# Performance work log

Hardware: AMD Instinct MI355X
Metric: run time of the kernel (lower is better)

The kernel has to match this reference:

```python
import jax, jax.numpy as jnp
import numpy as np

D = 256      # d_model
H = 8        # n_heads
L = 4        # n_levels
P = 4        # n_points
DFF = 1024   # d_ffn
DH = D // H  # head dim
SPATIAL = np.array([[100, 100], [50, 50], [25, 25], [13, 13]], dtype=np.int64)  # (H_l, W_l)
LV = int((SPATIAL[:, 0] * SPATIAL[:, 1]).sum())  # 13294 flattened memory tokens


def layer_norm(x, w, b, eps=1e-5):
    m = jnp.mean(x, -1, keepdims=True)
    v = jnp.mean((x - m) ** 2, -1, keepdims=True)
    return (x - m) * jax.lax.rsqrt(v + eps) * w + b


def setup_inputs() -> dict:
    key = jax.random.key(0)
    ks = jax.random.split(key, 16)
    nq, bs = 900, 8

    def w(k, shape, s=0.02):
        return jax.random.normal(k, shape, dtype=jnp.float32) * s

    return {
        "tgt": jax.random.normal(ks[0], (nq, bs, D), jnp.float32),
        "tgt_query_pos": jax.random.normal(ks[1], (nq, bs, D), jnp.float32),
        "tgt_reference_points": jax.random.uniform(ks[2], (nq, bs, L, 2), jnp.float32),
        "memory": jax.random.normal(ks[3], (LV, bs, D), jnp.float32),
        "sa_Wqkv": w(ks[4], (3 * D, D)), "sa_bqkv": jnp.zeros((3 * D,), jnp.float32),
        "sa_Wo": w(ks[5], (D, D)), "sa_bo": jnp.zeros((D,), jnp.float32),
        "ln1_w": jnp.ones((D,), jnp.float32), "ln1_b": jnp.zeros((D,), jnp.float32),
        "ln2_w": jnp.ones((D,), jnp.float32), "ln2_b": jnp.zeros((D,), jnp.float32),
        "ln3_w": jnp.ones((D,), jnp.float32), "ln3_b": jnp.zeros((D,), jnp.float32),
        "ca_Woff": w(ks[6], (H * L * P * 2, D)), "ca_boff": w(ks[7], (H * L * P * 2,), 0.5),
        "ca_Wattn": w(ks[8], (H * L * P, D)), "ca_battn": jnp.zeros((H * L * P,), jnp.float32),
        "ca_Wval": w(ks[9], (D, D)), "ca_bval": jnp.zeros((D,), jnp.float32),
        "ca_Wout": w(ks[10], (D, D)), "ca_bout": jnp.zeros((D,), jnp.float32),
        "ffn_W1": w(ks[11], (DFF, D)), "ffn_b1": jnp.zeros((DFF,), jnp.float32),
        "ffn_W2": w(ks[12], (D, DFF)), "ffn_b2": jnp.zeros((D,), jnp.float32),
        "memory_key_padding_mask": jnp.zeros((bs, LV), jnp.bool_),
        "memory_spatial_shapes": jnp.asarray(SPATIAL),
    }


def msdeform_attn(query, ref, value, mask, shapes_np,
                  Woff, boff, Wattn, battn, Wval, bval, Wout, bout):
    # query: [bs,nq,D], ref: [bs,nq,L,2], value: [bs,lv,D], mask: [bs,lv]
    bs, nq, _ = query.shape
    lv = value.shape[1]
    v = value @ Wval.T + bval
    v = jnp.where(mask[:, :, None], 0.0, v)
    v = v.reshape(bs, lv, H, DH).transpose(0, 2, 1, 3)  # [bs,H,lv,DH]
    off = (query @ Woff.T + boff).reshape(bs, nq, H, L, P, 2)
    aw = jax.nn.softmax((query @ Wattn.T + battn).reshape(bs, nq, H, L * P), -1)
    aw = aw.reshape(bs, nq, H, L, P)
    # offset normalizer is [W_l, H_l]
    norm = jnp.asarray(shapes_np[:, ::-1].copy(), jnp.float32)  # [L,2]
    loc = ref[:, :, None, :, None, :] + off / norm[None, None, None, :, None, :]
    out = jnp.zeros((bs, nq, H, DH), jnp.float32)
    start = 0
    for l in range(L):
        Hl, Wl = int(shapes_np[l, 0]), int(shapes_np[l, 1])
        vf = v[:, :, start:start + Hl * Wl]  # [bs,H,Hl*Wl,DH]
        start += Hl * Wl
        # grid_sample(align_corners=False) pixel coords
        x = loc[:, :, :, l, :, 0] * Wl - 0.5  # [bs,nq,H,P]
        y = loc[:, :, :, l, :, 1] * Hl - 0.5
        x0 = jnp.floor(x); y0 = jnp.floor(y)
        fx = x - x0; fy = y - y0
        x0i = x0.astype(jnp.int32); y0i = y0.astype(jnp.int32)

        def gather(yi, xi):
            valid = ((xi >= 0) & (xi < Wl) & (yi >= 0) & (yi < Hl)).astype(jnp.float32)
            idx = jnp.clip(yi, 0, Hl - 1) * Wl + jnp.clip(xi, 0, Wl - 1)
            idx_t = idx.transpose(0, 2, 1, 3).reshape(bs, H, nq * P, 1)
            g = jnp.take_along_axis(vf, idx_t, axis=2)  # [bs,H,nq*P,DH]
            return g * valid.transpose(0, 2, 1, 3).reshape(bs, H, nq * P, 1)

        def wgt(w):
            return w.transpose(0, 2, 1, 3).reshape(bs, H, nq * P, 1)

        samp = (gather(y0i, x0i) * wgt((1 - fx) * (1 - fy))
                + gather(y0i, x0i + 1) * wgt(fx * (1 - fy))
                + gather(y0i + 1, x0i) * wgt((1 - fx) * fy)
                + gather(y0i + 1, x0i + 1) * wgt(fx * fy))
        samp = samp.reshape(bs, H, nq, P, DH)
        out = out + jnp.einsum('bhqpd,bqhp->bqhd', samp, aw[:, :, :, l])
    return out.reshape(bs, nq, D) @ Wout.T + bout


def reference(tgt, tgt_query_pos, tgt_reference_points, memory,
              sa_Wqkv, sa_bqkv, sa_Wo, sa_bo,
              ln1_w, ln1_b, ln2_w, ln2_b, ln3_w, ln3_b,
              ca_Woff, ca_boff, ca_Wattn, ca_battn, ca_Wval, ca_bval, ca_Wout, ca_bout,
              ffn_W1, ffn_b1, ffn_W2, ffn_b2,
              memory_key_padding_mask, memory_spatial_shapes):
    shapes_np = np.asarray(memory_spatial_shapes)  # static per trace
    nq, bs, _ = tgt.shape
    # --- self attention (post-LN, residual) ---
    q = tgt + tgt_query_pos
    qp = (q @ sa_Wqkv[:D].T + sa_bqkv[:D]).reshape(nq, bs, H, DH)
    kp = (q @ sa_Wqkv[D:2 * D].T + sa_bqkv[D:2 * D]).reshape(nq, bs, H, DH)
    vp = (tgt @ sa_Wqkv[2 * D:].T + sa_bqkv[2 * D:]).reshape(nq, bs, H, DH)
    scores = jnp.einsum('qbhd,kbhd->bhqk', qp, kp) * (1.0 / float(np.sqrt(DH)))
    attn = jax.nn.softmax(scores, -1)
    o = jnp.einsum('bhqk,kbhd->qbhd', attn, vp).reshape(nq, bs, D) @ sa_Wo.T + sa_bo
    tgt = layer_norm(tgt + o, ln2_w, ln2_b)
    # --- multi-scale deformable cross attention ---
    query = (tgt + tgt_query_pos).transpose(1, 0, 2)      # [bs,nq,D]
    ref = tgt_reference_points.transpose(1, 0, 2, 3)      # [bs,nq,L,2]
    val = memory.transpose(1, 0, 2)                       # [bs,lv,D]
    ca = msdeform_attn(query, ref, val, memory_key_padding_mask, shapes_np,
                       ca_Woff, ca_boff, ca_Wattn, ca_battn,
                       ca_Wval, ca_bval, ca_Wout, ca_bout).transpose(1, 0, 2)
    tgt = layer_norm(tgt + ca, ln1_w, ln1_b)
    # --- FFN ---
    t2 = jax.nn.relu(tgt @ ffn_W1.T + ffn_b1) @ ffn_W2.T + ffn_b2
    return layer_norm(tgt + t2, ln3_w, ln3_b)
```

## Files before the change

kernel.cpp:

```cpp
#include <hip/hip_runtime.h>
#include <hip/hip_bf16.h>

#define NQ   900
#define BSZ  8
#define DM   256
#define NH   8
#define DHD  32
#define DFF_ 1024
#define LVTOT 13294
#define NTOK (NQ*BSZ)
#define MVAL (LVTOT*BSZ)

typedef __attribute__((ext_vector_type(8))) short bf16x8;
typedef __attribute__((ext_vector_type(4))) short bf16x4;
typedef __attribute__((ext_vector_type(4))) float f32x4;
typedef unsigned int u32;

__device__ __forceinline__ unsigned short f2bf(float x) {
  union { __hip_bfloat16 h; unsigned short u; } cv;
  cv.h = __float2bfloat16(x);
  return cv.u;
}
__device__ __forceinline__ float bf2f(unsigned short u) {
  union { __hip_bfloat16 h; unsigned short u; } cv;
  cv.u = u;
  return __bfloat162float(cv.h);
}

__device__ __forceinline__ void gl_lds16(const void* gsrc, void* ldst) {
  __builtin_amdgcn_global_load_lds(
      (const __attribute__((address_space(1))) u32*)gsrc,
      (__attribute__((address_space(3))) u32*)ldst, 16, 0, 0);
}

__global__ __launch_bounds__(256) void prep_kernel(
    const float* p0, const float* p1, const float* p2, const float* p3,
    const float* p4, const float* p5, const float* p6, const float* p7,
    unsigned short* wdst,
    const float* a, const float* b, unsigned short* qdst,
    const float* boff, const float* battn, float* bcat) {
  int bid = blockIdx.x, tid = threadIdx.x;
  if (bid < 496) {
    long i8 = ((long)bid * 256 + tid) * 8;
    const float* src; long off;
    if      (i8 < 196608) { src = p0; off = i8; }
    else if (i8 < 262144) { src = p1; off = i8 - 196608; }
    else if (i8 < 327680) { src = p2; off = i8 - 262144; }
    else if (i8 < 393216) { src = p3; off = i8 - 327680; }
    else if (i8 < 425984) { src = p4; off = i8 - 393216; }
    else if (i8 < 491520) { src = p5; off = i8 - 425984; }
    else if (i8 < 753664) { src = p6; off = i8 - 491520; }
    else                  { src = p7; off = i8 - 753664; }
    float4 x = *(const float4*)(src + off);
    float4 y = *(const float4*)(src + off + 4);
    bf16x8 v;
    v[0] = (short)f2bf(x.x); v[1] = (short)f2bf(x.y);
    v[2] = (short)f2bf(x.z); v[3] = (short)f2bf(x.w);
    v[4] = (short)f2bf(y.x); v[5] = (short)f2bf(y.y);
    v[6] = (short)f2bf(y.z); v[7] = (short)f2bf(y.w);
    *(bf16x8*)(wdst + i8) = v;
  } else if (bid < 496 + 900) {
    int i = (bid - 496) * 256 + tid;
    float4 a0 = ((const float4*)a)[i * 2], a1 = ((const float4*)a)[i * 2 + 1];
    float4 b0 = ((const float4*)b)[i * 2], b1 = ((const float4*)b)[i * 2 + 1];
    bf16x8 v;
    v[0] = (short)f2bf(a0.x + b0.x); v[1] = (short)f2bf(a0.y + b0.y);
    v[2] = (short)f2bf(a0.z + b0.z); v[3] = (short)f2bf(a0.w + b0.w);
    v[4] = (short)f2bf(a1.x + b1.x); v[5] = (short)f2bf(a1.y + b1.y);
    v[6] = (short)f2bf(a1.z + b1.z); v[7] = (short)f2bf(a1.w + b1.w);
    *(bf16x8*)(qdst + (long)i * 8) = v;
  } else {
    int i = (bid - 1396) * 256 + tid;
    if (i < 256) bcat[i] = boff[i];
    else if (i < 384) bcat[i] = battn[i - 256];
  }
}

struct B3 {
  const void* A[3];
  const unsigned short* W[3];
  const float* bias[3];
  void* C[3];
  int M[3], ldc[3], af32[3], blk0[3], nx[3];
};

__global__ __launch_bounds__(256, 4) void gemm_batch3_kernel(B3 ops) {
  constexpr int K = 256, NSTEP = 4;
  __shared__ alignas(16) unsigned char As[32768];
  __shared__ alignas(16) unsigned char Bs[16384];
  int bid = blockIdx.x;
  int oi = (bid >= ops.blk0[2]) ? 2 : (bid >= ops.blk0[1] ? 1 : 0);
  int rel = bid - ops.blk0[oi];
  int nx = ops.nx[oi];
  int bx = rel % nx, by = rel / nx;
  const void* Araw = ops.A[oi];
  const unsigned short* W = ops.W[oi];
  const float* bias = ops.bias[oi];
  void* C = ops.C[oi];
  int M = ops.M[oi], ldc = ops.ldc[oi], AF32 = ops.af32[oi];

  int tid = threadIdx.x;
  int l = tid & 63, w = tid >> 6;
  int lr = l & 15, lg = l >> 4;
  int wr = w >> 1, wc = w & 1;
  int n0 = bx * 128, m0 = by * 128;
  int phase = by & (NSTEP - 1);

  f32x4 acc[4][4];
#pragma unroll
  for (int m = 0; m < 4; m++)
#pragma unroll
    for (int n = 0; n < 4; n++) acc[m][n] = (f32x4){0.f, 0.f, 0.f, 0.f};

  for (int tt = 0; tt < NSTEP; tt++) {
    int t = tt + phase; if (t >= NSTEP) t -= NSTEP;
    int k0 = t * 64;
    __syncthreads();
#pragma unroll
    for (int i4 = 0; i4 < 4; i4++) {
      int i = i4 * 4 + w;
      int row = i * 8 + (l >> 3);
      int sc = (l & 7) ^ (row & 7);
      gl_lds16(W + (long)(n0 + row) * K + k0 + sc * 8, Bs + i * 1024 + l * 16);
    }
    if (AF32) {
      const float* Af = (const float*)Araw;
#pragma unroll
      for (int i4 = 0; i4 < 8; i4++) {
        int i = i4 * 4 + w;
        int row = i * 4 + (l >> 4);
        int g = m0 + row; if (g >= M) g = M - 1;
        int sc = (l & 15) ^ (row & 15);
        gl_lds16(Af + (long)g * K + k0 + sc * 4, As + i * 1024 + l * 16);
      }
    } else {
      const unsigned short* A = (const unsigned short*)Araw;
#pragma unroll
      for (int i4 = 0; i4 < 4; i4++) {
        int i = i4 * 4 + w;
        int row = i * 8 + (l >> 3);
        int g = m0 + row; if (g >= M) g = M - 1;
        int sc = (l & 7) ^ (row & 7);
        gl_lds16(A + (long)g * K + k0 + sc * 8, As + i * 1024 + l * 16);
      }
    }
    __syncthreads();
#pragma unroll
    for (int sk = 0; sk < 2; sk++) {
      bf16x8 af[4], bfr[4];
      if (AF32) {
#pragma unroll
        for (int m = 0; m < 4; m++) {
          int row = wr * 64 + m * 16 + lr;
          int ca = (sk * 8 + lg * 2) ^ (row & 15);
          int cb = (sk * 8 + lg * 2 + 1) ^ (row & 15);
          f32x4 fa = *(const f32x4*)(As + row * 256 + ca * 16);
          f32x4 fb = *(const f32x4*)(As + row * 256 + cb * 16);
          bf16x8 v;
          v[0] = (short)f2bf(fa[0]); v[1] = (short)f2bf(fa[1]);
          v[2] = (short)f2bf(fa[2]); v[3] = (short)f2bf(fa[3]);
          v[4] = (short)f2bf(fb[0]); v[5] = (short)f2bf(fb[1]);
          v[6] = (short)f2bf(fb[2]); v[7] = (short)f2bf(fb[3]);
          af[m] = v;
        }
      } else {
#pragma unroll
        for (int m = 0; m < 4; m++) {
          int row = wr * 64 + m * 16 + lr;
          int c = (sk * 4 + lg) ^ (row & 7);
          af[m] = *(const bf16x8*)(As + row * 128 + c * 16);
        }
      }
#pragma unroll
      for (int n = 0; n < 4; n++) {
        int row = wc * 64 + n * 16 + lr;
        int c = (sk * 4 + lg) ^ (row & 7);
        bfr[n] = *(const bf16x8*)(Bs + row * 128 + c * 16);
      }
#pragma unroll
      for (int m = 0; m < 4; m++)
#pragma unroll
        for (int n = 0; n < 4; n++)
          acc[m][n] = __builtin_amdgcn_mfma_f32_16x16x32_bf16(af[m], bfr[n], acc[m][n], 0, 0, 0);
    }
  }

  float bv[4];
#pragma unroll
  for (int ni = 0; ni < 4; ni++) bv[ni] = bias[n0 + wc * 64 + ni * 16 + lr];
#pragma unroll
  for (int mi = 0; mi < 4; mi++) {
#pragma unroll
    for (int r = 0; r < 4; r++) {
      int row = m0 + wr * 64 + mi * 16 + lg * 4 + r;
      if (row < M) {
#pragma unroll
        for (int ni = 0; ni < 4; ni++) {
          int col = n0 + wc * 64 + ni * 16 + lr;
          ((unsigned short*)C)[(long)row * ldc + col] = f2bf(acc[mi][ni][r] + bv[ni]);
        }
      }
    }
  }
}

template <int AF32, int OUT_BF16, int RELU, int NSTEP>
__global__ __launch_bounds__(256, 4) void gemm_s_kernel(
    const void* __restrict__ Araw, const unsigned short* __restrict__ W,
    const float* __restrict__ bias, void* __restrict__ C,
    int M, int ldc) {
  constexpr int K = NSTEP * 64;
  constexpr int ABYTES = AF32 ? 32768 : 16384;
  __shared__ alignas(16) unsigned char As[ABYTES];
  __shared__ alignas(16) unsigned char Bs[16384];
  int tid = threadIdx.x;
  int l = tid & 63, w = tid >> 6;
  int lr = l & 15, lg = l >> 4;
  int wr = w >> 1, wc = w & 1;
  int n0 = blockIdx.x * 128, m0 = blockIdx.y * 128;
  int phase = blockIdx.y & (NSTEP - 1);

  f32x4 acc[4][4];
#pragma unroll
  for (int m = 0; m < 4; m++)
#pragma unroll
    for (int n = 0; n < 4; n++) acc[m][n] = (f32x4){0.f, 0.f, 0.f, 0.f};

  for (int tt = 0; tt < NSTEP; tt++) {
    int t = tt + phase; if (t >= NSTEP) t -= NSTEP;
    int k0 = t * 64;
    __syncthreads();
#pragma unroll
    for (int i4 = 0; i4 < 4; i4++) {
      int i = i4 * 4 + w;
      int row = i * 8 + (l >> 3);
      int sc = (l & 7) ^ (row & 7);
      gl_lds16(W + (long)(n0 + row) * K + k0 + sc * 8, Bs + i * 1024 + l * 16);
    }
    if (AF32) {
      const float* Af = (const float*)Araw;
#pragma unroll
      for (int i4 = 0; i4 < 8; i4++) {
        int i = i4 * 4 + w;
        int row = i * 4 + (l >> 4);
        int g = m0 + row; if (g >= M) g = M - 1;
        int sc = (l & 15) ^ (row & 15);
        gl_lds16(Af + (long)g * K + k0 + sc * 4, As + i * 1024 + l * 16);
      }
    } else {
      const unsigned short* A = (const unsigned short*)Araw;
#pragma unroll
      for (int i4 = 0; i4 < 4; i4++) {
        int i = i4 * 4 + w;
        int row = i * 8 + (l >> 3);
        int g = m0 + row; if (g >= M) g = M - 1;
        int sc = (l & 7) ^ (row & 7);
        gl_lds16(A + (long)g * K + k0 + sc * 8, As + i * 1024 + l * 16);
      }
    }
    __syncthreads();
#pragma unroll
    for (int sk = 0; sk < 2; sk++) {
      bf16x8 af[4], bfr[4];
      if (AF32) {
#pragma unroll
        for (int m = 0; m < 4; m++) {
          int row = wr * 64 + m * 16 + lr;
          int ca = (sk * 8 + lg * 2) ^ (row & 15);
          int cb = (sk * 8 + lg * 2 + 1) ^ (row & 15);
          f32x4 fa = *(const f32x4*)(As + row * 256 + ca * 16);
          f32x4 fb = *(const f32x4*)(As + row * 256 + cb * 16);
          bf16x8 v;
          v[0] = (short)f2bf(fa[0]); v[1] = (short)f2bf(fa[1]);
          v[2] = (short)f2bf(fa[2]); v[3] = (short)f2bf(fa[3]);
          v[4] = (short)f2bf(fb[0]); v[5] = (short)f2bf(fb[1]);
          v[6] = (short)f2bf(fb[2]); v[7] = (short)f2bf(fb[3]);
          af[m] = v;
        }
      } else {
#pragma unroll
        for (int m = 0; m < 4; m++) {
          int row = wr * 64 + m * 16 + lr;
          int c = (sk * 4 + lg) ^ (row & 7);
          af[m] = *(const bf16x8*)(As + row * 128 + c * 16);
        }
      }
#pragma unroll
      for (int n = 0; n < 4; n++) {
        int row = wc * 64 + n * 16 + lr;
        int c = (sk * 4 + lg) ^ (row & 7);
        bfr[n] = *(const bf16x8*)(Bs + row * 128 + c * 16);
      }
#pragma unroll
      for (int m = 0; m < 4; m++)
#pragma unroll
        for (int n = 0; n < 4; n++)
          acc[m][n] = __builtin_amdgcn_mfma_f32_16x16x32_bf16(af[m], bfr[n], acc[m][n], 0, 0, 0);
    }
  }

  float bv[4];
#pragma unroll
  for (int ni = 0; ni < 4; ni++) bv[ni] = bias[n0 + wc * 64 + ni * 16 + lr];
#pragma unroll
  for (int mi = 0; mi < 4; mi++) {
#pragma unroll
    for (int r = 0; r < 4; r++) {
      int row = m0 + wr * 64 + mi * 16 + lg * 4 + r;
      if (row < M) {
#pragma unroll
        for (int ni = 0; ni < 4; ni++) {
          int col = n0 + wc * 64 + ni * 16 + lr;
          float v = acc[mi][ni][r] + bv[ni];
          if (RELU) v = fmaxf(v, 0.f);
          if (OUT_BF16) ((unsigned short*)C)[(long)row * ldc + col] = f2bf(v);
          else          ((float*)C)[(long)row * ldc + col] = v;
        }
      }
    }
  }
}

__global__ __launch_bounds__(256) void attn_mfma_kernel(const unsigned short* __restrict__ qkv,
                                                        unsigned short* __restrict__ out) {
  __shared__ unsigned short Vt[32][72];
  __shared__ unsigned short Ps[4][16][72];
  int tid = threadIdx.x;
  int l = tid & 63, w = tid >> 6;
  int lr = l & 15, lg = l >> 4;
  int bid = blockIdx.x;
  int xcd = bid & 7;
  int rest = bid >> 3;
  int pgrp = rest / 15;
  int qt   = rest - pgrp * 15;
  int pair = pgrp * 8 + xcd;
  int q0 = qt * 64;
  int h = pair & 7, b = pair >> 3;
  const float scale = 0.17677669529663687f;

  int qrow = q0 + w * 16 + lr;
  int qclamp = qrow < 899 ? qrow : 899;
  bf16x8 qf = *(const bf16x8*)(qkv + ((long)qclamp * 8 + b) * 768 + h * 32 + lg * 8);

  f32x4 o_acc[2];
  o_acc[0] = (f32x4){0.f, 0.f, 0.f, 0.f};
  o_acc[1] = (f32x4){0.f, 0.f, 0.f, 0.f};
  float m_run[4] = {-1e30f, -1e30f, -1e30f, -1e30f};
  float l_run[4] = {0.f, 0.f, 0.f, 0.f};

  for (int k0 = 0; k0 < NQ; k0 += 64) {
    __syncthreads();
    {
      int key = tid >> 2, dg = tid & 3;
      int kk = k0 + key; if (kk > 899) kk = 899;
      bf16x8 vv = *(const bf16x8*)(qkv + ((long)kk * 8 + b) * 768 + 512 + h * 32 + dg * 8);
#pragma unroll
      for (int j = 0; j < 8; j++) Vt[dg * 8 + j][key] = (unsigned short)vv[j];
    }
    f32x4 sg[4];
#pragma unroll
    for (int ng = 0; ng < 4; ng++) {
      int key = k0 + ng * 16 + lr; int kc = key < 899 ? key : 899;
      bf16x8 kf = *(const bf16x8*)(qkv + ((long)kc * 8 + b) * 768 + 256 + h * 32 + lg * 8);
      sg[ng] = __builtin_amdgcn_mfma_f32_16x16x32_bf16(qf, kf, (f32x4){0.f, 0.f, 0.f, 0.f}, 0, 0, 0);
    }
    float sv[4][4];
#pragma unroll
    for (int ng = 0; ng < 4; ng++) {
      bool bad = (k0 + ng * 16 + lr) >= NQ;
#pragma unroll
      for (int r = 0; r < 4; r++) sv[ng][r] = bad ? -1e30f : sg[ng][r] * scale;
    }
    float p[4][4];
#pragma unroll
    for (int r = 0; r < 4; r++) {
      float rmax = fmaxf(fmaxf(sv[0][r], sv[1][r]), fmaxf(sv[2][r], sv[3][r]));
#pragma unroll
      for (int mk = 8; mk; mk >>= 1) rmax = fmaxf(rmax, __shfl_xor(rmax, mk));
      float mnew = fmaxf(m_run[r], rmax);
      float fs = __expf(m_run[r] - mnew);
      m_run[r] = mnew;
      float ps = 0.f;
#pragma unroll
      for (int ng = 0; ng < 4; ng++) { p[ng][r] = __expf(sv[ng][r] - mnew); ps += p[ng][r]; }
#pragma unroll
      for (int mk = 8; mk; mk >>= 1) ps += __shfl_xor(ps, mk);
      l_run[r] = l_run[r] * fs + ps;
      o_acc[0][r] *= fs;
      o_acc[1][r] *= fs;
    }
#pragma unroll
    for (int ng = 0; ng < 4; ng++)
#pragma unroll
      for (int r = 0; r < 4; r++)
        Ps[w][lg * 4 + r][lr + ng * 16] = f2bf(p[ng][r]);
    __syncthreads();
#pragma unroll
    for (int ks = 0; ks < 2; ks++) {
      bf16x8 pf = *(const bf16x8*)&Ps[w][lr][ks * 32 + lg * 8];
#pragma unroll
      for (int ni = 0; ni < 2; ni++) {
        bf16x8 vf = *(const bf16x8*)&Vt[ni * 16 + lr][ks * 32 + lg * 8];
        o_acc[ni] = __builtin_amdgcn_mfma_f32_16x16x32_bf16(pf, vf, o_acc[ni], 0, 0, 0);
      }
    }
  }
#pragma unroll
  for (int r = 0; r < 4; r++) {
    int orow = q0 + w * 16 + lg * 4 + r;
    if (orow < NQ) {
      float inv = 1.f / l_run[r];
      unsigned short* op = out + ((long)orow * 8 + b) * 256 + h * 32 + lr;
      op[0]  = f2bf(o_acc[0][r] * inv);
      op[16] = f2bf(o_acc[1][r] * inv);
    }
  }
}

__device__ __forceinline__ void fetch16_acc(const unsigned short* __restrict__ vtmp, int lo, int W,
                                            int yi, int xi, int b, int col0, float wgt,
                                            float* a) {
  if ((xi < 0) | (xi >= W) | (yi < 0) | (yi >= W)) return;
  const unsigned short* p = vtmp + ((long)((lo + yi * W + xi) * BSZ + b)) * 256 + col0;
  bf16x8 r0 = *(const bf16x8*)p;
  bf16x8 r1 = *(const bf16x8*)(p + 8);
#pragma unroll
  for (int j = 0; j < 8; j++) a[j] += wgt * bf2f((unsigned short)r0[j]);
#pragma unroll
  for (int j = 0; j < 8; j++) a[8 + j] += wgt * bf2f((unsigned short)r1[j]);
}

__global__ __launch_bounds__(256) void sampler_kernel(const unsigned short* __restrict__ vtmp,
                                                      const float* __restrict__ oa,
                                                      const float* __restrict__ ref,
                                                      unsigned short* __restrict__ samp) {
  __shared__ float s_off[16][256];
  __shared__ float s_aw[16][128];
  __shared__ float s_ref[16][8];
  int tid = threadIdx.x;
  int bid = blockIdx.x;
  int img = bid & 7;
  int jb  = bid >> 3;
  int qi0 = jb * 16;
#pragma unroll
  for (int k = 0; k < 16; k++) {
    int qi = qi0 + k; if (qi > 899) qi = 899;
    long t = (long)qi * 8 + img;
    s_off[k][tid] = oa[t * 384 + tid];
  }
#pragma unroll
  for (int i = 0; i < 8; i++) {
    int idx = i * 256 + tid;
    int k = idx >> 7, c = idx & 127;
    int qi = qi0 + k; if (qi > 899) qi = 899;
    long t = (long)qi * 8 + img;
    s_aw[k][c] = oa[t * 384 + 256 + c];
  }
  if (tid < 128) {
    int k = tid >> 3;
    int qi = qi0 + k; if (qi > 899) qi = 899;
    long t = (long)qi * 8 + img;
    s_ref[k][tid & 7] = ref[t * 8 + (tid & 7)];
  }
  __syncthreads();
  if (tid < 128) {
    int k = tid >> 3, hh = tid & 7;
    float* p = &s_aw[k][hh * 16];
    float m = -1e30f;
#pragma unroll
    for (int j = 0; j < 16; j++) m = fmaxf(m, p[j]);
    float s = 0.f;
#pragma unroll
    for (int j = 0; j < 16; j++) { p[j] = __expf(p[j] - m); s += p[j]; }
    float inv = 1.f / s;
#pragma unroll
    for (int j = 0; j < 16; j++) p[j] *= inv;
  }
  __syncthreads();
  int w = tid >> 4;
  int l = tid & 15;
  int qi = qi0 + w;
  int h = l >> 1, col0 = h * 32 + (l & 1) * 16;
  int b = img;
  const int Wls[4]  = {100, 50, 25, 13};
  const int lofs[4] = {0, 10000, 12500, 13125};
  float a[16];
#pragma unroll
  for (int j = 0; j < 16; j++) a[j] = 0.f;
#pragma unroll
  for (int lvl = 0; lvl < 4; lvl++) {
    int W = Wls[lvl];
    float Wf = (float)W;
    int lo = lofs[lvl];
    float rx = s_ref[w][lvl * 2 + 0], ry = s_ref[w][lvl * 2 + 1];
#pragma unroll
    for (int p = 0; p < 4; p++) {
      float ox = s_off[w][((h * 4 + lvl) * 4 + p) * 2 + 0];
      float oy = s_off[w][((h * 4 + lvl) * 4 + p) * 2 + 1];
      float x = rx * Wf + ox - 0.5f;
      float y = ry * Wf + oy - 0.5f;
      float x0f = floorf(x), y0f = floorf(y);
      float fx = x - x0f, fy = y - y0f;
      int x0 = (int)x0f, y0 = (int)y0f;
      float aa = s_aw[w][h * 16 + lvl * 4 + p];
      float w00 = aa * (1.f - fx) * (1.f - fy);
      float w01 = aa * fx * (1.f - fy);
      float w10 = aa * (1.f - fx) * fy;
      float w11 = aa * fx * fy;
      fetch16_acc(vtmp, lo, W, y0,     x0,     b, col0, w00, a);
      fetch16_acc(vtmp, lo, W, y0,     x0 + 1, b, col0, w01, a);
      fetch16_acc(vtmp, lo, W, y0 + 1, x0,     b, col0, w10, a);
      fetch16_acc(vtmp, lo, W, y0 + 1, x0 + 1, b, col0, w11, a);
    }
  }
  if (qi < NQ) {
    long t = (long)qi * 8 + img;
    bf16x8 o0, o1;
#pragma unroll
    for (int j = 0; j < 8; j++) { o0[j] = (short)f2bf(a[j]); o1[j] = (short)f2bf(a[8 + j]); }
    *(bf16x8*)(samp + t * 256 + col0) = o0;
    *(bf16x8*)(samp + t * 256 + col0 + 8) = o1;
  }
}

__global__ __launch_bounds__(256) void ln_kernel(const float* __restrict__ x,
                                                 const float* __restrict__ res,
                                                 const float* __restrict__ w,
                                                 const float* __restrict__ bvec,
                                                 float* __restrict__ out,
                                                 unsigned short* __restrict__ out_bf,
                                                 const float* __restrict__ pos,
                                                 unsigned short* __restrict__ pos_bf,
                                                 int rows) {
  int wv = threadIdx.x >> 6, lane = threadIdx.x & 63;
  int row = blockIdx.x * 4 + wv;
  if (row >= rows) return;
  float4 xv = *(const float4*)(x + (long)row * 256 + lane * 4);
  float4 rv = *(const float4*)(res + (long)row * 256 + lane * 4);
  float v0 = xv.x + rv.x, v1 = xv.y + rv.y, v2 = xv.z + rv.z, v3 = xv.w + rv.w;
  float s = v0 + v1 + v2 + v3;
#pragma unroll
  for (int o = 32; o; o >>= 1) s += __shfl_xor(s, o);
  float mean = s * (1.f / 256.f);
  float d0 = v0 - mean, d1 = v1 - mean, d2 = v2 - mean, d3 = v3 - mean;
  float q = d0 * d0 + d1 * d1 + d2 * d2 + d3 * d3;
#pragma unroll
  for (int o = 32; o; o >>= 1) q += __shfl_xor(q, o);
  float rstd = rsqrtf(q * (1.f / 256.f) + 1e-5f);
  float4 wv4 = *(const float4*)(w + lane * 4);
  float4 bv4 = *(const float4*)(bvec + lane * 4);
  float o0 = d0 * rstd * wv4.x + bv4.x;
  float o1 = d1 * rstd * wv4.y + bv4.y;
  float o2 = d2 * rstd * wv4.z + bv4.z;
  float o3 = d3 * rstd * wv4.w + bv4.w;
  *(float4*)(out + (long)row * 256 + lane * 4) = make_float4(o0, o1, o2, o3);
  if (out_bf) {
    unsigned short* p = out_bf + (long)row * 256 + lane * 4;
    p[0] = f2bf(o0); p[1] = f2bf(o1); p[2] = f2bf(o2); p[3] = f2bf(o3);
  }
  if (pos_bf) {
    float4 pv = *(const float4*)(pos + (long)row * 256 + lane * 4);
    unsigned short* p = pos_bf + (long)row * 256 + lane * 4;
    p[0] = f2bf(o0 + pv.x); p[1] = f2bf(o1 + pv.y);
    p[2] = f2bf(o2 + pv.z); p[3] = f2bf(o3 + pv.w);
  }
}

extern "C" void kernel_launch(void* const* d_in, const int* in_sizes, int n_in,
                              void* d_out, int out_size, void* d_ws, size_t ws_size,
                              hipStream_t stream) {
  const float* tgt     = (const float*)d_in[0];
  const float* pos     = (const float*)d_in[1];
  const float* refpts  = (const float*)d_in[2];
  const float* memory  = (const float*)d_in[3];
  const float* sa_Wqkv = (const float*)d_in[4];
  const float* sa_bqkv = (const float*)d_in[5];
  const float* sa_Wo   = (const float*)d_in[6];
  const float* sa_bo   = (const float*)d_in[7];
  const float* ln1_w   = (const float*)d_in[8];
  const float* ln1_b   = (const float*)d_in[9];
  const float* ln2_w   = (const float*)d_in[10];
  const float* ln2_b   = (const float*)d_in[11];
  const float* ln3_w   = (const float*)d_in[12];
  const float* ln3_b   = (const float*)d_in[13];
  const float* ca_Woff = (const float*)d_in[14];
  const float* ca_boff = (const float*)d_in[15];
  const float* ca_Wattn= (const float*)d_in[16];
  const float* ca_battn= (const float*)d_in[17];
  const float* ca_Wval = (const float*)d_in[18];
  const float* ca_bval = (const float*)d_in[19];
  const float* ca_Wout = (const float*)d_in[20];
  const float* ca_bout = (const float*)d_in[21];
  const float* ffn_W1  = (const float*)d_in[22];
  const float* ffn_b1  = (const float*)d_in[23];
  const float* ffn_W2  = (const float*)d_in[24];
  const float* ffn_b2  = (const float*)d_in[25];

  char* ws = (char*)d_ws;
  float*          buf_ca = (float*)(ws);
  float*          buf_t3 = (float*)(ws + 8388608);
  unsigned short* t3_bf  = (unsigned short*)(ws + 16777216);
  unsigned short* buf_h  = (unsigned short*)(ws + 20971520);
  float*          buf_f  = (float*)(ws + 36700160);
  float*          bias_cat = (float*)(ws + 44072960);
  unsigned short* buf_v  = (unsigned short*)(ws + 54452224);
  unsigned short* wts    = (unsigned short*)(ws + 112590848);
  unsigned short* buf_q  = (unsigned short*)(ws + 114622464);
  unsigned short* buf_qkv= (unsigned short*)(ws + 118308864);
  float*          buf_oa = (float*)(ws + 118308864);
  unsigned short* buf_o  = (unsigned short*)(ws + 129368064);
  unsigned short* buf_smp= (unsigned short*)(ws + 129368064);
  float*          buf_t2 = (float*)(ws + 133054464);

  const unsigned short* w_qkv = wts + 0;
  const unsigned short* w_o   = wts + 196608;
  const unsigned short* w_val = wts + 262144;
  const unsigned short* w_oa  = wts + 327680;
  const unsigned short* w_out = wts + 425984;
  const unsigned short* w_f1  = wts + 491520;
  const unsigned short* w_f2  = wts + 753664;

  dim3 blk(256);

  prep_kernel<<<1398, blk, 0, stream>>>(sa_Wqkv, sa_Wo, ca_Wval, ca_Woff, ca_Wattn,
                                        ca_Wout, ffn_W1, ffn_W2, wts,
                                        tgt, pos, buf_q, ca_boff, ca_battn, bias_cat);

  B3 ops;
  ops.A[0] = memory;   ops.W[0] = w_val;           ops.bias[0] = ca_bval;      ops.C[0] = buf_v;
  ops.M[0] = MVAL;     ops.ldc[0] = 256;           ops.af32[0] = 1;            ops.nx[0] = 2;
  ops.A[1] = buf_q;    ops.W[1] = w_qkv;           ops.bias[1] = sa_bqkv;      ops.C[1] = buf_qkv;
  ops.M[1] = NTOK;     ops.ldc[1] = 768;           ops.af32[1] = 0;            ops.nx[1] = 4;
  ops.A[2] = tgt;      ops.W[2] = w_qkv + 512*256; ops.bias[2] = sa_bqkv + 512; ops.C[2] = buf_qkv + 512;
  ops.M[2] = NTOK;     ops.ldc[2] = 768;           ops.af32[2] = 1;            ops.nx[2] = 2;
  ops.blk0[0] = 0; ops.blk0[1] = 1662; ops.blk0[2] = 1890;
  gemm_batch3_kernel<<<2004, blk, 0, stream>>>(ops);

  attn_mfma_kernel<<<960, blk, 0, stream>>>(buf_qkv, buf_o);
  gemm_s_kernel<0, 0, 0, 4><<<dim3(2, 57), blk, 0, stream>>>(buf_o, w_o, sa_bo,
                                                             buf_t2, NTOK, 256);
  ln_kernel<<<1800, blk, 0, stream>>>(buf_t2, tgt, ln2_w, ln2_b, buf_t2, nullptr,
                                      pos, buf_q, NTOK);
  gemm_s_kernel<0, 0, 0, 4><<<dim3(3, 57), blk, 0, stream>>>(buf_q, w_oa, bias_cat,
                                                             buf_oa, NTOK, 384);
  sampler_kernel<<<456, blk, 0, stream>>>(buf_v, buf_oa, refpts, buf_smp);
  gemm_s_kernel<0, 0, 0, 4><<<dim3(2, 57), blk, 0, stream>>>(buf_smp, w_out, ca_bout,
                                                             buf_ca, NTOK, 256);
  ln_kernel<<<1800, blk, 0, stream>>>(buf_ca, buf_t2, ln1_w, ln1_b, buf_t3, t3_bf,
                                      nullptr, nullptr, NTOK);
  gemm_s_kernel<0, 1, 1, 4><<<dim3(8, 57), blk, 0, stream>>>(t3_bf, w_f1, ffn_b1,
                                                             buf_h, NTOK, 1024);
  gemm_s_kernel<0, 0, 0, 16><<<dim3(2, 57), blk, 0, stream>>>(buf_h, w_f2, ffn_b2,
                                                              buf_f, NTOK, 256);
  ln_kernel<<<1800, blk, 0, stream>>>(buf_f, buf_t3, ln3_w, ln3_b, (float*)d_out, nullptr,
                                      nullptr, nullptr, NTOK);
}
```

Baseline: 213.6 us.

## Fuse value projection GEMM with self-attention into one heterogeneous launch

The large memory value-projection GEMM moves out of the batched QKV GEMM launch into a new combined kernel. Its first 1662 blocks run the value GEMM and the remaining 960 blocks run the self-attention, which does not depend on it. The batched launch shrinks to just the Q/K and V projections, so attention can start sooner and overlap with the big value GEMM instead of waiting behind it. The cost is a shared 48KB LDS footprint for attention blocks, which may reduce their occupancy, and block scheduling order now decides how much overlap actually happens.

Result: slower. 221.9 us (+3.9%).

```diff
diff --git a/kernel.cpp b/kernel.cpp
--- a/kernel.cpp
+++ b/kernel.cpp
@@ -204,6 +204,192 @@
   }
 }
 
+#define NVB 1662
+__global__ __launch_bounds__(256, 4) void value_attn_kernel(
+    const float* __restrict__ memory, const unsigned short* __restrict__ Wv,
+    const float* __restrict__ bval, unsigned short* __restrict__ Cv,
+    const unsigned short* __restrict__ qkv, unsigned short* __restrict__ out) {
+  __shared__ alignas(16) unsigned char smem[49152];
+  int tid = threadIdx.x;
+  int l = tid & 63, w = tid >> 6;
+  int lr = l & 15, lg = l >> 4;
+
+  if (blockIdx.x < NVB) {
+    constexpr int K = 256, NSTEP = 4;
+    unsigned char* As = smem;
+    unsigned char* Bs = smem + 32768;
+    int wr = w >> 1, wc = w & 1;
+    int bx = blockIdx.x & 1, by = blockIdx.x >> 1;
+    int n0 = bx * 128, m0 = by * 128;
+    int phase = by & (NSTEP - 1);
+
+    f32x4 acc[4][4];
+#pragma unroll
+    for (int m = 0; m < 4; m++)
+#pragma unroll
+      for (int n = 0; n < 4; n++) acc[m][n] = (f32x4){0.f, 0.f, 0.f, 0.f};
+
+    for (int tt = 0; tt < NSTEP; tt++) {
+      int t = tt + phase; if (t >= NSTEP) t -= NSTEP;
+      int k0 = t * 64;
+      __syncthreads();
+#pragma unroll
+      for (int i4 = 0; i4 < 4; i4++) {
+        int i = i4 * 4 + w;
+        int row = i * 8 + (l >> 3);
+        int sc = (l & 7) ^ (row & 7);
+        gl_lds16(Wv + (long)(n0 + row) * K + k0 + sc * 8, Bs + i * 1024 + l * 16);
+      }
+#pragma unroll
+      for (int i4 = 0; i4 < 8; i4++) {
+        int i = i4 * 4 + w;
+        int row = i * 4 + (l >> 4);
+        int g = m0 + row; if (g >= MVAL) g = MVAL - 1;
+        int sc = (l & 15) ^ (row & 15);
+        gl_lds16(memory + (long)g * K + k0 + sc * 4, As + i * 1024 + l * 16);
+      }
+      __syncthreads();
+#pragma unroll
+      for (int sk = 0; sk < 2; sk++) {
+        bf16x8 af[4], bfr[4];
+#pragma unroll
+        for (int m = 0; m < 4; m++) {
+          int row = wr * 64 + m * 16 + lr;
+          int ca = (sk * 8 + lg * 2) ^ (row & 15);
+          int cb = (sk * 8 + lg * 2 + 1) ^ (row & 15);
+          f32x4 fa = *(const f32x4*)(As + row * 256 + ca * 16);
+          f32x4 fb = *(const f32x4*)(As + row * 256 + cb * 16);
+          bf16x8 v;
+          v[0] = (short)f2bf(fa[0]); v[1] = (short)f2bf(fa[1]);
+          v[2] = (short)f2bf(fa[2]); v[3] = (short)f2bf(fa[3]);
+          v[4] = (short)f2bf(fb[0]); v[5] = (short)f2bf(fb[1]);
+          v[6] = (short)f2bf(fb[2]); v[7] = (short)f2bf(fb[3]);
+          af[m] = v;
+        }
+#pragma unroll
+        for (int n = 0; n < 4; n++) {
+          int row = wc * 64 + n * 16 + lr;
+          int c = (sk * 4 + lg) ^ (row & 7);
+          bfr[n] = *(const bf16x8*)(Bs + row * 128 + c * 16);
+        }
+#pragma unroll
+        for (int m = 0; m < 4; m++)
+#pragma unroll
+          for (int n = 0; n < 4; n++)
+            acc[m][n] = __builtin_amdgcn_mfma_f32_16x16x32_bf16(af[m], bfr[n], acc[m][n], 0, 0, 0);
+      }
+    }
+
+    float bv[4];
+#pragma unroll
+    for (int ni = 0; ni < 4; ni++) bv[ni] = bval[n0 + wc * 64 + ni * 16 + lr];
+#pragma unroll
+    for (int mi = 0; mi < 4; mi++) {
+#pragma unroll
+      for (int r = 0; r < 4; r++) {
+        int row = m0 + wr * 64 + mi * 16 + lg * 4 + r;
+        if (row < MVAL) {
+#pragma unroll
+          for (int ni = 0; ni < 4; ni++) {
+            int col = n0 + wc * 64 + ni * 16 + lr;
+            Cv[(long)row * 256 + col] = f2bf(acc[mi][ni][r] + bv[ni]);
+          }
+        }
+      }
+    }
+  } else {
+    unsigned short (*Vt)[72] = (unsigned short(*)[72])smem;
+    unsigned short (*Ps)[16][72] = (unsigned short(*)[16][72])(smem + 4608);
+    int bid = blockIdx.x - NVB;
+    int xcd = bid & 7;
+    int rest = bid >> 3;
+    int pgrp = rest / 15;
+    int qt   = rest - pgrp * 15;
+    int pair = pgrp * 8 + xcd;
+    int q0 = qt * 64;
+    int h = pair & 7, b = pair >> 3;
+    const float scale = 0.17677669529663687f;
+
+    int qrow = q0 + w * 16 + lr;
+    int qclamp = qrow < 899 ? qrow : 899;
+    bf16x8 qf = *(const bf16x8*)(qkv + ((long)qclamp * 8 + b) * 768 + h * 32 + lg * 8);
+
+    f32x4 o_acc[2];
+    o_acc[0] = (f32x4){0.f, 0.f, 0.f, 0.f};
+    o_acc[1] = (f32x4){0.f, 0.f, 0.f, 0.f};
+    float m_run[4] = {-1e30f, -1e30f, -1e30f, -1e30f};
+    float l_run[4] = {0.f, 0.f, 0.f, 0.f};
+
+    for (int k0 = 0; k0 < NQ; k0 += 64) {
+      __syncthreads();
+      {
+        int key = tid >> 2, dg = tid & 3;
+        int kk = k0 + key; if (kk > 899) kk = 899;
+        bf16x8 vv = *(const bf16x8*)(qkv + ((long)kk * 8 + b) * 768 + 512 + h * 32 + dg * 8);
+#pragma unroll
+        for (int j = 0; j < 8; j++) Vt[dg * 8 + j][key] = (unsigned short)vv[j];
+      }
+      f32x4 sg[4];
+#pragma unroll
+      for (int ng = 0; ng < 4; ng++) {
+        int key = k0 + ng * 16 + lr; int kc = key < 899 ? key : 899;
+        bf16x8 kf = *(const bf16x8*)(qkv + ((long)kc * 8 + b) * 768 + 256 + h * 32 + lg * 8);
+        sg[ng] = __builtin_amdgcn_mfma_f32_16x16x32_bf16(qf, kf, (f32x4){0.f, 0.f, 0.f, 0.f}, 0, 0, 0);
+      }
+      float sv[4][4];
+#pragma unroll
+      for (int ng = 0; ng < 4; ng++) {
+        bool bad = (k0 + ng * 16 + lr) >= NQ;
+#pragma unroll
+        for (int r = 0; r < 4; r++) sv[ng][r] = bad ? -1e30f : sg[ng][r] * scale;
+      }
+      float p[4][4];
+#pragma unroll
+      for (int r = 0; r < 4; r++) {
+        float rmax = fmaxf(fmaxf(sv[0][r], sv[1][r]), fmaxf(sv[2][r], sv[3][r]));
+#pragma unroll
+        for (int mk = 8; mk; mk >>= 1) rmax = fmaxf(rmax, __shfl_xor(rmax, mk));
+        float mnew = fmaxf(m_run[r], rmax);
+        float fs = __expf(m_run[r] - mnew);
+        m_run[r] = mnew;
+        float ps = 0.f;
+#pragma unroll
+        for (int ng = 0; ng < 4; ng++) { p[ng][r] = __expf(sv[ng][r] - mnew); ps += p[ng][r]; }
+#pragma unroll
+        for (int mk = 8; mk; mk >>= 1) ps += __shfl_xor(ps, mk);
+        l_run[r] = l_run[r] * fs + ps;
+        o_acc[0][r] *= fs;
+        o_acc[1][r] *= fs;
+      }
+#pragma unroll
+      for (int ng = 0; ng < 4; ng++)
+#pragma unroll
+        for (int r = 0; r < 4; r++)
+          Ps[w][lg * 4 + r][lr + ng * 16] = f2bf(p[ng][r]);
+      __syncthreads();
+#pragma unroll
+      for (int ks = 0; ks < 2; ks++) {
+        bf16x8 pf = *(const bf16x8*)&Ps[w][lr][ks * 32 + lg * 8];
+#pragma unroll
+        for (int ni = 0; ni < 2; ni++) {
+          bf16x8 vf = *(const bf16x8*)&Vt[ni * 16 + lr][ks * 32 + lg * 8];
+          o_acc[ni] = __builtin_amdgcn_mfma_f32_16x16x32_bf16(pf, vf, o_acc[ni], 0, 0, 0);
+        }
+      }
+    }
+#pragma unroll
+    for (int r = 0; r < 4; r++) {
+      int orow = q0 + w * 16 + lg * 4 + r;
+      if (orow < NQ) {
+        float inv = 1.f / l_run[r];
+        unsigned short* op = out + ((long)orow * 8 + b) * 256 + h * 32 + lr;
+        op[0]  = f2bf(o_acc[0][r] * inv);
+        op[16] = f2bf(o_acc[1][r] * inv);
+      }
+    }
+  }
+}
+
 template <int AF32, int OUT_BF16, int RELU, int NSTEP>
 __global__ __launch_bounds__(256, 4) void gemm_s_kernel(
     const void* __restrict__ Araw, const unsigned short* __restrict__ W,
@@ -317,102 +503,6 @@
           else          ((float*)C)[(long)row * ldc + col] = v;
         }
       }
-    }
-  }
-}
-
-__global__ __launch_bounds__(256) void attn_mfma_kernel(const unsigned short* __restrict__ qkv,
-                                                        unsigned short* __restrict__ out) {
-  __shared__ unsigned short Vt[32][72];
-  __shared__ unsigned short Ps[4][16][72];
-  int tid = threadIdx.x;
-  int l = tid & 63, w = tid >> 6;
-  int lr = l & 15, lg = l >> 4;
-  int bid = blockIdx.x;
-  int xcd = bid & 7;
-  int rest = bid >> 3;
-  int pgrp = rest / 15;
-  int qt   = rest - pgrp * 15;
-  int pair = pgrp * 8 + xcd;
-  int q0 = qt * 64;
-  int h = pair & 7, b = pair >> 3;
-  const float scale = 0.17677669529663687f;
-
-  int qrow = q0 + w * 16 + lr;
-  int qclamp = qrow < 899 ? qrow : 899;
-  bf16x8 qf = *(const bf16x8*)(qkv + ((long)qclamp * 8 + b) * 768 + h * 32 + lg * 8);
-
-  f32x4 o_acc[2];
-  o_acc[0] = (f32x4){0.f, 0.f, 0.f, 0.f};
-  o_acc[1] = (f32x4){0.f, 0.f, 0.f, 0.f};
-  float m_run[4] = {-1e30f, -1e30f, -1e30f, -1e30f};
-  float l_run[4] = {0.f, 0.f, 0.f, 0.f};
-
-  for (int k0 = 0; k0 < NQ; k0 += 64) {
-    __syncthreads();
-    {
-      int key = tid >> 2, dg = tid & 3;
-      int kk = k0 + key; if (kk > 899) kk = 899;
-      bf16x8 vv = *(const bf16x8*)(qkv + ((long)kk * 8 + b) * 768 + 512 + h * 32 + dg * 8);
-#pragma unroll
-      for (int j = 0; j < 8; j++) Vt[dg * 8 + j][key] = (unsigned short)vv[j];
-    }
-    f32x4 sg[4];
-#pragma unroll
-    for (int ng = 0; ng < 4; ng++) {
-      int key = k0 + ng * 16 + lr; int kc = key < 899 ? key : 899;
-      bf16x8 kf = *(const bf16x8*)(qkv + ((long)kc * 8 + b) * 768 + 256 + h * 32 + lg * 8);
-      sg[ng] = __builtin_amdgcn_mfma_f32_16x16x32_bf16(qf, kf, (f32x4){0.f, 0.f, 0.f, 0.f}, 0, 0, 0);
-    }
-    float sv[4][4];
-#pragma unroll
-    for (int ng = 0; ng < 4; ng++) {
-      bool bad = (k0 + ng * 16 + lr) >= NQ;
-#pragma unroll
-      for (int r = 0; r < 4; r++) sv[ng][r] = bad ? -1e30f : sg[ng][r] * scale;
-    }
-    float p[4][4];
-#pragma unroll
-    for (int r = 0; r < 4; r++) {
-      float rmax = fmaxf(fmaxf(sv[0][r], sv[1][r]), fmaxf(sv[2][r], sv[3][r]));
-#pragma unroll
-      for (int mk = 8; mk; mk >>= 1) rmax = fmaxf(rmax, __shfl_xor(rmax, mk));
-      float mnew = fmaxf(m_run[r], rmax);
-      float fs = __expf(m_run[r] - mnew);
-      m_run[r] = mnew;
-      float ps = 0.f;
-#pragma unroll
-      for (int ng = 0; ng < 4; ng++) { p[ng][r] = __expf(sv[ng][r] - mnew); ps += p[ng][r]; }
-#pragma unroll
-      for (int mk = 8; mk; mk >>= 1) ps += __shfl_xor(ps, mk);
-      l_run[r] = l_run[r] * fs + ps;
-      o_acc[0][r] *= fs;
-      o_acc[1][r] *= fs;
-    }
-#pragma unroll
-    for (int ng = 0; ng < 4; ng++)
-#pragma unroll
-      for (int r = 0; r < 4; r++)
-        Ps[w][lg * 4 + r][lr + ng * 16] = f2bf(p[ng][r]);
-    __syncthreads();
-#pragma unroll
-    for (int ks = 0; ks < 2; ks++) {
-      bf16x8 pf = *(const bf16x8*)&Ps[w][lr][ks * 32 + lg * 8];
-#pragma unroll
-      for (int ni = 0; ni < 2; ni++) {
-        bf16x8 vf = *(const bf16x8*)&Vt[ni * 16 + lr][ks * 32 + lg * 8];
-        o_acc[ni] = __builtin_amdgcn_mfma_f32_16x16x32_bf16(pf, vf, o_acc[ni], 0, 0, 0);
-      }
-    }
-  }
-#pragma unroll
-  for (int r = 0; r < 4; r++) {
-    int orow = q0 + w * 16 + lg * 4 + r;
-    if (orow < NQ) {
-      float inv = 1.f / l_run[r];
-      unsigned short* op = out + ((long)orow * 8 + b) * 256 + h * 32 + lr;
-      op[0]  = f2bf(o_acc[0][r] * inv);
-      op[16] = f2bf(o_acc[1][r] * inv);
     }
   }
 }
@@ -627,16 +717,18 @@
                                         tgt, pos, buf_q, ca_boff, ca_battn, bias_cat);
 
   B3 ops;
-  ops.A[0] = memory;   ops.W[0] = w_val;           ops.bias[0] = ca_bval;      ops.C[0] = buf_v;
-  ops.M[0] = MVAL;     ops.ldc[0] = 256;           ops.af32[0] = 1;            ops.nx[0] = 2;
+  ops.A[0] = buf_q;    ops.W[0] = w_qkv;           ops.bias[0] = sa_bqkv;      ops.C[0] = buf_qkv;
+  ops.M[0] = NTOK;     ops.ldc[0] = 768;           ops.af32[0] = 0;            ops.nx[0] = 4;
   ops.A[1] = buf_q;    ops.W[1] = w_qkv;           ops.bias[1] = sa_bqkv;      ops.C[1] = buf_qkv;
   ops.M[1] = NTOK;     ops.ldc[1] = 768;           ops.af32[1] = 0;            ops.nx[1] = 4;
   ops.A[2] = tgt;      ops.W[2] = w_qkv + 512*256; ops.bias[2] = sa_bqkv + 512; ops.C[2] = buf_qkv + 512;
   ops.M[2] = NTOK;     ops.ldc[2] = 768;           ops.af32[2] = 1;            ops.nx[2] = 2;
-  ops.blk0[0] = 0; ops.blk0[1] = 1662; ops.blk0[2] = 1890;
-  gemm_batch3_kernel<<<2004, blk, 0, stream>>>(ops);
-
-  attn_mfma_kernel<<<960, blk, 0, stream>>>(buf_qkv, buf_o);
+  ops.blk0[0] = 0; ops.blk0[1] = 0; ops.blk0[2] = 228;
+  gemm_batch3_kernel<<<342, blk, 0, stream>>>(ops);
+
+  value_attn_kernel<<<NVB + 960, blk, 0, stream>>>(memory, w_val, ca_bval, buf_v,
+                                                   buf_qkv, buf_o);
+
   gemm_s_kernel<0, 0, 0, 4><<<dim3(2, 57), blk, 0, stream>>>(buf_o, w_o, sa_bo,
                                                              buf_t2, NTOK, 256);
   ln_kernel<<<1800, blk, 0, stream>>>(buf_t2, tgt, ln2_w, ln2_b, buf_t2, nullptr,
```
